# Performance work log

Measured on AMD Instinct MI355X. Metric: run time of the kernel, lower is better.

## Reference

```python
import jax, jax.numpy as jnp
import numpy as np

NUM_HEADS = 4


def setup_inputs() -> dict:
    key = jax.random.key(0)
    ks = jax.random.split(key, 5)
    B, C, L = 8, 128, 2048
    x = jax.random.normal(ks[0], (B, C, L), dtype=jnp.float32)
    # Conv1d(C, 3C, 1) == per-position linear; weight [3C, C], bias [3C]
    w_qkv = jax.random.normal(ks[1], (3 * C, C), dtype=jnp.float32) * (1.0 / np.sqrt(C))
    b_qkv = jax.random.normal(ks[2], (3 * C,), dtype=jnp.float32) * 0.01
    w_proj = jax.random.normal(ks[3], (C, C), dtype=jnp.float32) * (1.0 / np.sqrt(C))
    b_proj = jax.random.normal(ks[4], (C,), dtype=jnp.float32) * 0.01
    return {"x": x, "w_qkv": w_qkv, "b_qkv": b_qkv, "w_proj": w_proj, "b_proj": b_proj}


def reference(x, w_qkv, b_qkv, w_proj, b_proj):
    B, C, L = x.shape
    H = NUM_HEADS
    D = C // H
    scale = D ** -0.5
    # 1x1 conv qkv projection: [B, 3C, L]
    qkv = jnp.einsum('oc,bcl->bol', w_qkv, x) + b_qkv[None, :, None]
    # reshape (B,3,H,D,L) -> permute to (3,B,H,L,D)
    qkv = qkv.reshape(B, 3, H, D, L).transpose(1, 0, 2, 4, 3)
    q, k, v = qkv[0], qkv[1], qkv[2]  # each [B, H, L, D]
    attn = jax.nn.softmax(jnp.einsum('bhld,bhmd->bhlm', q, k) * scale, axis=-1)
    out = jnp.einsum('bhlm,bhmd->bhld', attn, v)  # [B, H, L, D]
    out = out.transpose(0, 1, 3, 2).reshape(B, C, L)
    out = jnp.einsum('oc,bcl->bol', w_proj, out) + b_proj[None, :, None]
    return out + x
```

## Files before the change

kernel.cpp:

```cpp
#include <hip/hip_runtime.h>

#define Bsz 8
#define Cdim 128
#define Lseq 2048
#define NH 4
#define HD 32
#define BH 32
#define QSCALE (0.17677669529663687f * 1.4426950408889634f)

typedef __bf16 bf16x8 __attribute__((ext_vector_type(8)));
typedef float f32x4 __attribute__((ext_vector_type(4)));
typedef unsigned u32x4 __attribute__((ext_vector_type(4)));

__device__ __forceinline__ float fexp2(float x) {
#if __has_builtin(__builtin_amdgcn_exp2f)
    return __builtin_amdgcn_exp2f(x);
#else
    return __expf(x * 0.6931471805599453f);
#endif
}

__device__ __forceinline__ unsigned short f2bf(float f) {
    unsigned u = __builtin_bit_cast(unsigned, f);
    u += 0x7FFFu + ((u >> 16) & 1u);
    return (unsigned short)(u >> 16);
}

__device__ __forceinline__ unsigned pack_bf16(float a, float b) {
    return (unsigned)f2bf(a) | ((unsigned)f2bf(b) << 16);
}

__device__ __forceinline__ unsigned pack_bf16_rtz(float a, float b) {
    return __builtin_amdgcn_perm(__builtin_bit_cast(unsigned, b),
                                 __builtin_bit_cast(unsigned, a), 0x07060302u);
}

__device__ __forceinline__ float bf_lo(unsigned u) {
    return __builtin_bit_cast(float, u << 16);
}
__device__ __forceinline__ float bf_hi(unsigned u) {
    return __builtin_bit_cast(float, u & 0xFFFF0000u);
}

#define MFMA16(A, B, C) __builtin_amdgcn_mfma_f32_16x16x32_bf16((A), (B), (C), 0, 0, 0)

__global__ __launch_bounds__(256) void qkv_kernel(const float* __restrict__ x,
        const float* __restrict__ w, const float* __restrict__ bias,
        unsigned short* __restrict__ qh, unsigned short* __restrict__ kh,
        unsigned short* __restrict__ vh) {
    __shared__ __attribute__((aligned(16))) unsigned short T[64][132];
    int bid = blockIdx.x;
    int og3 = bid % 3;
    int lt  = (bid / 3) & 31;
    int b   = bid / 96;
    int l0 = lt * 64;
    int t = threadIdx.x;
    int lane = t & 63, wv = t >> 6;
    int m16 = lane & 15, quad = lane >> 4;

    bf16x8 af[2][4];
    float bs[2][4];
    #pragma unroll
    for (int os = 0; os < 2; os++) {
        int orow = og3 * 128 + os * 64 + wv * 16;
        #pragma unroll
        for (int ks = 0; ks < 4; ks++) {
            const float* p = w + (size_t)(orow + m16) * Cdim + ks * 32 + quad * 8;
            float4 f0 = *(const float4*)p;
            float4 f1 = *(const float4*)(p + 4);
            u32x4 u = {pack_bf16(f0.x, f0.y), pack_bf16(f0.z, f0.w),
                       pack_bf16(f1.x, f1.y), pack_bf16(f1.z, f1.w)};
            af[os][ks] = __builtin_bit_cast(bf16x8, u);
        }
        #pragma unroll
        for (int r = 0; r < 4; r++) bs[os][r] = bias[orow + quad * 4 + r];
    }

    {
        int ll = t & 63, cg = t >> 6;
        const float* xb = x + (size_t)b * Cdim * Lseq + l0 + ll;
        #pragma unroll
        for (int i = 0; i < 16; i++) {
            int c = cg * 32 + 2 * i;
            float f0 = xb[(size_t)c * Lseq];
            float f1 = xb[(size_t)(c + 1) * Lseq];
            *(unsigned*)&T[ll][c] = pack_bf16(f0, f1);
        }
    }
    __syncthreads();

    #pragma unroll
    for (int ns = 0; ns < 4; ns++) {
        bf16x8 bx[4];
        #pragma unroll
        for (int ks = 0; ks < 4; ks++)
            bx[ks] = *(const bf16x8*)(&T[ns * 16 + m16][ks * 32 + quad * 8]);
        int l = l0 + ns * 16 + m16;
        #pragma unroll
        for (int os = 0; os < 2; os++) {
            f32x4 acc = {0.f, 0.f, 0.f, 0.f};
            #pragma unroll
            for (int ks = 0; ks < 4; ks++) acc = MFMA16(af[os][ks], bx[ks], acc);
            int oq = os * 64 + wv * 16 + quad * 4;
            if (og3 == 0) {
                int h = oq >> 5, d0 = oq & 31;
                uint2 u;
                u.x = pack_bf16((acc[0] + bs[os][0]) * QSCALE, (acc[1] + bs[os][1]) * QSCALE);
                u.y = pack_bf16((acc[2] + bs[os][2]) * QSCALE, (acc[3] + bs[os][3]) * QSCALE);
                *(uint2*)(qh + ((size_t)(b * NH + h) * Lseq + l) * HD + d0) = u;
            } else if (og3 == 1) {
                int h = oq >> 5, d0 = oq & 31;
                uint2 u;
                u.x = pack_bf16(acc[0] + bs[os][0], acc[1] + bs[os][1]);
                u.y = pack_bf16(acc[2] + bs[os][2], acc[3] + bs[os][3]);
                *(uint2*)(kh + ((size_t)(b * NH + h) * Lseq + l) * HD + d0) = u;
            } else {
                int kc = l >> 6, kk = l & 63;
                int half = kk >> 5, k32 = kk & 31;
                int q_, j_;
                if (k32 < 16) { q_ = k32 >> 2; j_ = k32 & 3; }
                else          { q_ = (k32 - 16) >> 2; j_ = 4 + ((k32 - 16) & 3); }
                int pos = half * 32 + q_ * 8 + j_;
                #pragma unroll
                for (int r = 0; r < 4; r++) {
                    int o = oq + r, h = o >> 5, d = o & 31;
                    vh[(((size_t)(b * NH + h) * 32 + kc) * HD + d) * 64 + pos] =
                        f2bf(acc[r] + bs[os][r]);
                }
            }
        }
    }
}

__global__ __launch_bounds__(256) void attn_kernel(
        const unsigned short* __restrict__ qh, const unsigned short* __restrict__ kh,
        const unsigned short* __restrict__ vh, unsigned short* __restrict__ oo) {
    __shared__ __attribute__((aligned(16))) char smem[22528];

    int bid = blockIdx.x;
    int xcd  = bid & 7;
    int rest = bid >> 3;
    int qt = rest & 31;
    int g  = rest >> 5;
    int bh = xcd + 8 * g;

    int lane = threadIdx.x & 63;
    int wv   = threadIdx.x >> 6;
    int m16  = lane & 15;
    int quad = lane >> 4;
    int l0 = qt * 64;

    bf16x8 qf[4];
    #pragma unroll
    for (int qs = 0; qs < 4; qs++)
        qf[qs] = *(const bf16x8*)(qh + ((size_t)bh * Lseq + l0 + qs * 16 + m16) * HD + quad * 8);

    f32x4 oacc[4][2];
    float sacc[4];
    #pragma unroll
    for (int qs = 0; qs < 4; qs++) {
        oacc[qs][0] = f32x4{0.f, 0.f, 0.f, 0.f};
        oacc[qs][1] = f32x4{0.f, 0.f, 0.f, 0.f};
        sacc[qs]    = 0.f;
    }
    f32x4 zero = {0.f, 0.f, 0.f, 0.f};

    const unsigned short* kb = kh + (size_t)bh * Lseq * HD + m16 * HD + quad * 8;
    const unsigned short* vb = vh + (size_t)bh * 32 * HD * 64;
    int kbase = wv * 512;

    auto load_kv = [&](int chunk, bf16x8* kf, bf16x8* vf) {
        int k0 = kbase + chunk * 64;
        #pragma unroll
        for (int t = 0; t < 4; t++)
            kf[t] = *(const bf16x8*)(kb + (size_t)(k0 + 16 * t) * HD);
        const unsigned short* vch = vb + (size_t)(k0 >> 6) * (HD * 64);
        vf[0] = *(const bf16x8*)(vch + m16 * 64 + quad * 8);
        vf[1] = *(const bf16x8*)(vch + (16 + m16) * 64 + quad * 8);
        vf[2] = *(const bf16x8*)(vch + m16 * 64 + 32 + quad * 8);
        vf[3] = *(const bf16x8*)(vch + (16 + m16) * 64 + 32 + quad * 8);
    };

    auto compute = [&](const bf16x8* kf, const bf16x8* vf) {
        #pragma unroll
        for (int qs = 0; qs < 4; qs++) {
            f32x4 s0 = MFMA16(kf[0], qf[qs], zero);
            f32x4 s1 = MFMA16(kf[1], qf[qs], zero);
            f32x4 s2 = MFMA16(kf[2], qf[qs], zero);
            f32x4 s3 = MFMA16(kf[3], qf[qs], zero);
            float p00 = fexp2(s0[0]), p01 = fexp2(s0[1]), p02 = fexp2(s0[2]), p03 = fexp2(s0[3]);
            float p10 = fexp2(s1[0]), p11 = fexp2(s1[1]), p12 = fexp2(s1[2]), p13 = fexp2(s1[3]);
            float p20 = fexp2(s2[0]), p21 = fexp2(s2[1]), p22 = fexp2(s2[2]), p23 = fexp2(s2[3]);
            float p30 = fexp2(s3[0]), p31 = fexp2(s3[1]), p32 = fexp2(s3[2]), p33 = fexp2(s3[3]);
            float r0 = (p00 + p01) + (p02 + p03);
            float r1 = (p10 + p11) + (p12 + p13);
            float r2 = (p20 + p21) + (p22 + p23);
            float r3 = (p30 + p31) + (p32 + p33);
            sacc[qs] += (r0 + r1) + (r2 + r3);
            u32x4 lo = {pack_bf16_rtz(p00, p01), pack_bf16_rtz(p02, p03),
                        pack_bf16_rtz(p10, p11), pack_bf16_rtz(p12, p13)};
            u32x4 hi = {pack_bf16_rtz(p20, p21), pack_bf16_rtz(p22, p23),
                        pack_bf16_rtz(p30, p31), pack_bf16_rtz(p32, p33)};
            bf16x8 pfL = __builtin_bit_cast(bf16x8, lo);
            bf16x8 pfH = __builtin_bit_cast(bf16x8, hi);
            oacc[qs][0] = MFMA16(vf[0], pfL, oacc[qs][0]);
            oacc[qs][1] = MFMA16(vf[1], pfL, oacc[qs][1]);
            oacc[qs][0] = MFMA16(vf[2], pfH, oacc[qs][0]);
            oacc[qs][1] = MFMA16(vf[3], pfH, oacc[qs][1]);
        }
    };

    bf16x8 kA[4], vA[4], kB[4], vB[4];
    load_kv(0, kA, vA);
    load_kv(1, kB, vB);
    compute(kA, vA); load_kv(2, kA, vA);
    compute(kB, vB); load_kv(3, kB, vB);
    compute(kA, vA); load_kv(4, kA, vA);
    compute(kB, vB); load_kv(5, kB, vB);
    compute(kA, vA); load_kv(6, kA, vA);
    compute(kB, vB); load_kv(7, kB, vB);
    compute(kA, vA);
    compute(kB, vB);

    unsigned* red_o = (unsigned*)smem;
    float* red_l = (float*)(smem + 18432);
    #pragma unroll
    for (int qs = 0; qs < 4; qs++) {
        int row = qs * 16 + m16;
        unsigned* rw = red_o + (size_t)(wv * 64 + row) * 18;
        *(uint2*)(rw + 2 * quad) =
            make_uint2(pack_bf16_rtz(oacc[qs][0][0], oacc[qs][0][1]),
                       pack_bf16_rtz(oacc[qs][0][2], oacc[qs][0][3]));
        *(uint2*)(rw + 8 + 2 * quad) =
            make_uint2(pack_bf16_rtz(oacc[qs][1][0], oacc[qs][1][1]),
                       pack_bf16_rtz(oacc[qs][1][2], oacc[qs][1][3]));
        red_l[(wv * 64 + row) * 4 + quad] = sacc[qs];
    }
    __syncthreads();

    int q = threadIdx.x >> 2;
    int s4 = (threadIdx.x & 3) * 4;
    float a8[8] = {0.f, 0.f, 0.f, 0.f, 0.f, 0.f, 0.f, 0.f};
    float lt = 0.f;
    #pragma unroll
    for (int w = 0; w < 4; w++) {
        const unsigned* rr = red_o + (size_t)(w * 64 + q) * 18 + s4;
        uint2 ua = *(const uint2*)(rr);
        uint2 ub = *(const uint2*)(rr + 2);
        a8[0] += bf_lo(ua.x); a8[1] += bf_hi(ua.x);
        a8[2] += bf_lo(ua.y); a8[3] += bf_hi(ua.y);
        a8[4] += bf_lo(ub.x); a8[5] += bf_hi(ub.x);
        a8[6] += bf_lo(ub.y); a8[7] += bf_hi(ub.y);
        float4 lv = *(const float4*)(red_l + (size_t)(w * 64 + q) * 4);
        lt += (lv.x + lv.y) + (lv.z + lv.w);
    }
    float inv = 1.0f / lt;
    int d0 = (threadIdx.x & 3) * 8;
    uint4 u;
    u.x = pack_bf16(a8[0] * inv, a8[1] * inv);
    u.y = pack_bf16(a8[2] * inv, a8[3] * inv);
    u.z = pack_bf16(a8[4] * inv, a8[5] * inv);
    u.w = pack_bf16(a8[6] * inv, a8[7] * inv);
    *(uint4*)(oo + ((size_t)bh * Lseq + l0 + q) * HD + d0) = u;
}

__global__ __launch_bounds__(256) void proj_kernel(const float* __restrict__ wp,
        const unsigned short* __restrict__ oo, const float* __restrict__ bias,
        const float* __restrict__ x, float* __restrict__ out) {
    int bid = blockIdx.x;
    int ot = bid & 1;
    int nt = bid >> 1;
    int n0 = nt * 32;
    int t = threadIdx.x;
    int lane = t & 63;
    int wv = t >> 6;
    int m16 = lane & 15, quad = lane >> 4;
    int o0 = ot * 64 + wv * 16;

    bf16x8 af[4];
    #pragma unroll
    for (int ks = 0; ks < 4; ks++) {
        const float* p = wp + (size_t)(o0 + m16) * Cdim + ks * 32 + quad * 8;
        float4 f0 = *(const float4*)p;
        float4 f1 = *(const float4*)(p + 4);
        u32x4 u = {pack_bf16(f0.x, f0.y), pack_bf16(f0.z, f0.w),
                   pack_bf16(f1.x, f1.y), pack_bf16(f1.z, f1.w)};
        af[ks] = __builtin_bit_cast(bf16x8, u);
    }
    float bs[4];
    #pragma unroll
    for (int r = 0; r < 4; r++) bs[r] = bias[o0 + quad * 4 + r];
    int oq = o0 + quad * 4;

    #pragma unroll
    for (int lt2 = 0; lt2 < 2; lt2++) {
        int n = n0 + lt2 * 16 + m16;
        int b = n >> 11, l = n & (Lseq - 1);
        bf16x8 bx[4];
        #pragma unroll
        for (int ks = 0; ks < 4; ks++)
            bx[ks] = *(const bf16x8*)(oo + ((size_t)(b * NH + ks) * Lseq + l) * HD + quad * 8);
        f32x4 acc = {0.f, 0.f, 0.f, 0.f};
        #pragma unroll
        for (int ks = 0; ks < 4; ks++) acc = MFMA16(af[ks], bx[ks], acc);
        #pragma unroll
        for (int r = 0; r < 4; r++) {
            size_t xi = ((size_t)b * Cdim + oq + r) * Lseq + l;
            out[xi] = acc[r] + bs[r] + x[xi];
        }
    }
}

extern "C" void kernel_launch(void* const* d_in, const int* in_sizes, int n_in,
                              void* d_out, int out_size, void* d_ws, size_t ws_size,
                              hipStream_t stream) {
    const float* x      = (const float*)d_in[0];
    const float* w_qkv  = (const float*)d_in[1];
    const float* b_qkv  = (const float*)d_in[2];
    const float* w_proj = (const float*)d_in[3];
    const float* b_proj = (const float*)d_in[4];
    float* out = (float*)d_out;

    const size_t E = (size_t)BH * Lseq * HD;
    unsigned short* qh = (unsigned short*)d_ws;
    unsigned short* kh = qh + E;
    unsigned short* vh = kh + E;
    unsigned short* oo = vh + E;

    qkv_kernel<<<dim3(768), dim3(256), 0, stream>>>(x, w_qkv, b_qkv, qh, kh, vh);
    attn_kernel<<<dim3(1024), dim3(256), 0, stream>>>(qh, kh, vh, oo);
    proj_kernel<<<dim3(1024), dim3(256), 0, stream>>>(w_proj, oo, b_proj, x, out);
}
```

Before: 114.9 us.

## Double attention query tile to 128 rows and remap qkv blocks across XCDs

Each attention block now handles 128 query rows instead of 64. Every K/V fragment loaded from global memory feeds twice as many score and PV MFMAs, which halves the grid to 512 blocks. The cross-wave reduction buffer grows to 48KB, and launch_bounds(256,2) is added to hold occupancy despite doubled accumulator registers. The qkv kernel's block index is also remapped so the three output groups for a tile sit on the same XCD, for L2 locality. The risks are register pressure or spills, and fewer blocks to fill the CUs.

```diff
diff --git a/kernel.cpp b/kernel.cpp
--- a/kernel.cpp
+++ b/kernel.cpp
@@ -50,9 +50,13 @@
         unsigned short* __restrict__ vh) {
     __shared__ __attribute__((aligned(16))) unsigned short T[64][132];
     int bid = blockIdx.x;
-    int og3 = bid % 3;
-    int lt  = (bid / 3) & 31;
-    int b   = bid / 96;
+    int xcd = bid & 7;
+    int s   = bid >> 3;
+    int og3 = s % 3;
+    int u_  = s / 3;
+    int trio = u_ * 8 + xcd;
+    int lt  = trio & 31;
+    int b   = trio >> 5;
     int l0 = lt * 64;
     int t = threadIdx.x;
     int lane = t & 63, wv = t >> 6;
@@ -132,37 +136,42 @@
     }
 }
 
-__global__ __launch_bounds__(256) void attn_kernel(
+__global__ __launch_bounds__(256, 2) void attn_kernel(
         const unsigned short* __restrict__ qh, const unsigned short* __restrict__ kh,
         const unsigned short* __restrict__ vh, unsigned short* __restrict__ oo) {
-    __shared__ __attribute__((aligned(16))) char smem[22528];
+    __shared__ __attribute__((aligned(16))) char smem[49152];
 
     int bid = blockIdx.x;
     int xcd  = bid & 7;
     int rest = bid >> 3;
-    int qt = rest & 31;
-    int g  = rest >> 5;
+    int qt = rest & 15;
+    int g  = rest >> 4;
     int bh = xcd + 8 * g;
 
     int lane = threadIdx.x & 63;
     int wv   = threadIdx.x >> 6;
     int m16  = lane & 15;
     int quad = lane >> 4;
-    int l0 = qt * 64;
-
-    bf16x8 qf[4];
-    #pragma unroll
-    for (int qs = 0; qs < 4; qs++)
-        qf[qs] = *(const bf16x8*)(qh + ((size_t)bh * Lseq + l0 + qs * 16 + m16) * HD + quad * 8);
-
-    f32x4 oacc[4][2];
-    float sacc[4];
-    #pragma unroll
-    for (int qs = 0; qs < 4; qs++) {
-        oacc[qs][0] = f32x4{0.f, 0.f, 0.f, 0.f};
-        oacc[qs][1] = f32x4{0.f, 0.f, 0.f, 0.f};
-        sacc[qs]    = 0.f;
-    }
+    int l0 = qt * 128;
+
+    bf16x8 qf[2][4];
+    #pragma unroll
+    for (int qt2 = 0; qt2 < 2; qt2++)
+        #pragma unroll
+        for (int qs = 0; qs < 4; qs++)
+            qf[qt2][qs] = *(const bf16x8*)(
+                qh + ((size_t)bh * Lseq + l0 + qt2 * 64 + qs * 16 + m16) * HD + quad * 8);
+
+    f32x4 oacc[2][4][2];
+    float sacc[2][4];
+    #pragma unroll
+    for (int qt2 = 0; qt2 < 2; qt2++)
+        #pragma unroll
+        for (int qs = 0; qs < 4; qs++) {
+            oacc[qt2][qs][0] = f32x4{0.f, 0.f, 0.f, 0.f};
+            oacc[qt2][qs][1] = f32x4{0.f, 0.f, 0.f, 0.f};
+            sacc[qt2][qs]    = 0.f;
+        }
     f32x4 zero = {0.f, 0.f, 0.f, 0.f};
 
     const unsigned short* kb = kh + (size_t)bh * Lseq * HD + m16 * HD + quad * 8;
@@ -183,30 +192,33 @@
 
     auto compute = [&](const bf16x8* kf, const bf16x8* vf) {
         #pragma unroll
-        for (int qs = 0; qs < 4; qs++) {
-            f32x4 s0 = MFMA16(kf[0], qf[qs], zero);
-            f32x4 s1 = MFMA16(kf[1], qf[qs], zero);
-            f32x4 s2 = MFMA16(kf[2], qf[qs], zero);
-            f32x4 s3 = MFMA16(kf[3], qf[qs], zero);
-            float p00 = fexp2(s0[0]), p01 = fexp2(s0[1]), p02 = fexp2(s0[2]), p03 = fexp2(s0[3]);
-            float p10 = fexp2(s1[0]), p11 = fexp2(s1[1]), p12 = fexp2(s1[2]), p13 = fexp2(s1[3]);
-            float p20 = fexp2(s2[0]), p21 = fexp2(s2[1]), p22 = fexp2(s2[2]), p23 = fexp2(s2[3]);
-            float p30 = fexp2(s3[0]), p31 = fexp2(s3[1]), p32 = fexp2(s3[2]), p33 = fexp2(s3[3]);
-            float r0 = (p00 + p01) + (p02 + p03);
-            float r1 = (p10 + p11) + (p12 + p13);
-            float r2 = (p20 + p21) + (p22 + p23);
-            float r3 = (p30 + p31) + (p32 + p33);
-            sacc[qs] += (r0 + r1) + (r2 + r3);
-            u32x4 lo = {pack_bf16_rtz(p00, p01), pack_bf16_rtz(p02, p03),
-                        pack_bf16_rtz(p10, p11), pack_bf16_rtz(p12, p13)};
-            u32x4 hi = {pack_bf16_rtz(p20, p21), pack_bf16_rtz(p22, p23),
-                        pack_bf16_rtz(p30, p31), pack_bf16_rtz(p32, p33)};
-            bf16x8 pfL = __builtin_bit_cast(bf16x8, lo);
-            bf16x8 pfH = __builtin_bit_cast(bf16x8, hi);
-            oacc[qs][0] = MFMA16(vf[0], pfL, oacc[qs][0]);
-            oacc[qs][1] = MFMA16(vf[1], pfL, oacc[qs][1]);
-            oacc[qs][0] = MFMA16(vf[2], pfH, oacc[qs][0]);
-            oacc[qs][1] = MFMA16(vf[3], pfH, oacc[qs][1]);
+        for (int qt2 = 0; qt2 < 2; qt2++) {
+            #pragma unroll
+            for (int qs = 0; qs < 4; qs++) {
+                f32x4 s0 = MFMA16(kf[0], qf[qt2][qs], zero);
+                f32x4 s1 = MFMA16(kf[1], qf[qt2][qs], zero);
+                f32x4 s2 = MFMA16(kf[2], qf[qt2][qs], zero);
+                f32x4 s3 = MFMA16(kf[3], qf[qt2][qs], zero);
+                float p00 = fexp2(s0[0]), p01 = fexp2(s0[1]), p02 = fexp2(s0[2]), p03 = fexp2(s0[3]);
+                float p10 = fexp2(s1[0]), p11 = fexp2(s1[1]), p12 = fexp2(s1[2]), p13 = fexp2(s1[3]);
+                float p20 = fexp2(s2[0]), p21 = fexp2(s2[1]), p22 = fexp2(s2[2]), p23 = fexp2(s2[3]);
+                float p30 = fexp2(s3[0]), p31 = fexp2(s3[1]), p32 = fexp2(s3[2]), p33 = fexp2(s3[3]);
+                float r0 = (p00 + p01) + (p02 + p03);
+                float r1 = (p10 + p11) + (p12 + p13);
+                float r2 = (p20 + p21) + (p22 + p23);
+                float r3 = (p30 + p31) + (p32 + p33);
+                sacc[qt2][qs] += (r0 + r1) + (r2 + r3);
+                u32x4 lo = {pack_bf16_rtz(p00, p01), pack_bf16_rtz(p02, p03),
+                            pack_bf16_rtz(p10, p11), pack_bf16_rtz(p12, p13)};
+                u32x4 hi = {pack_bf16_rtz(p20, p21), pack_bf16_rtz(p22, p23),
+                            pack_bf16_rtz(p30, p31), pack_bf16_rtz(p32, p33)};
+                bf16x8 pfL = __builtin_bit_cast(bf16x8, lo);
+                bf16x8 pfH = __builtin_bit_cast(bf16x8, hi);
+                oacc[qt2][qs][0] = MFMA16(vf[0], pfL, oacc[qt2][qs][0]);
+                oacc[qt2][qs][1] = MFMA16(vf[1], pfL, oacc[qt2][qs][1]);
+                oacc[qt2][qs][0] = MFMA16(vf[2], pfH, oacc[qt2][qs][0]);
+                oacc[qt2][qs][1] = MFMA16(vf[3], pfH, oacc[qt2][qs][1]);
+            }
         }
     };
 
@@ -223,45 +235,59 @@
     compute(kB, vB);
 
     unsigned* red_o = (unsigned*)smem;
-    float* red_l = (float*)(smem + 18432);
-    #pragma unroll
-    for (int qs = 0; qs < 4; qs++) {
-        int row = qs * 16 + m16;
-        unsigned* rw = red_o + (size_t)(wv * 64 + row) * 18;
-        *(uint2*)(rw + 2 * quad) =
-            make_uint2(pack_bf16_rtz(oacc[qs][0][0], oacc[qs][0][1]),
-                       pack_bf16_rtz(oacc[qs][0][2], oacc[qs][0][3]));
-        *(uint2*)(rw + 8 + 2 * quad) =
-            make_uint2(pack_bf16_rtz(oacc[qs][1][0], oacc[qs][1][1]),
-                       pack_bf16_rtz(oacc[qs][1][2], oacc[qs][1][3]));
-        red_l[(wv * 64 + row) * 4 + quad] = sacc[qs];
-    }
+    float* red_l = (float*)(smem + 40960);
+    #pragma unroll
+    for (int qt2 = 0; qt2 < 2; qt2++)
+        #pragma unroll
+        for (int qs = 0; qs < 4; qs++) {
+            int row = qt2 * 64 + qs * 16 + m16;
+            unsigned* rw = red_o + (size_t)(wv * 128 + row) * 20;
+            *(uint2*)(rw + 2 * quad) =
+                make_uint2(pack_bf16_rtz(oacc[qt2][qs][0][0], oacc[qt2][qs][0][1]),
+                           pack_bf16_rtz(oacc[qt2][qs][0][2], oacc[qt2][qs][0][3]));
+            *(uint2*)(rw + 8 + 2 * quad) =
+                make_uint2(pack_bf16_rtz(oacc[qt2][qs][1][0], oacc[qt2][qs][1][1]),
+                           pack_bf16_rtz(oacc[qt2][qs][1][2], oacc[qt2][qs][1][3]));
+            red_l[(wv * 128 + row) * 4 + quad] = sacc[qt2][qs];
+        }
     __syncthreads();
 
-    int q = threadIdx.x >> 2;
-    int s4 = (threadIdx.x & 3) * 4;
-    float a8[8] = {0.f, 0.f, 0.f, 0.f, 0.f, 0.f, 0.f, 0.f};
-    float lt = 0.f;
+    int q = threadIdx.x >> 1;
+    int hcol = threadIdx.x & 1;
+    int s8 = hcol * 8;
+    float a16[16];
+    #pragma unroll
+    for (int i = 0; i < 16; i++) a16[i] = 0.f;
+    float ltot = 0.f;
     #pragma unroll
     for (int w = 0; w < 4; w++) {
-        const unsigned* rr = red_o + (size_t)(w * 64 + q) * 18 + s4;
-        uint2 ua = *(const uint2*)(rr);
-        uint2 ub = *(const uint2*)(rr + 2);
-        a8[0] += bf_lo(ua.x); a8[1] += bf_hi(ua.x);
-        a8[2] += bf_lo(ua.y); a8[3] += bf_hi(ua.y);
-        a8[4] += bf_lo(ub.x); a8[5] += bf_hi(ub.x);
-        a8[6] += bf_lo(ub.y); a8[7] += bf_hi(ub.y);
-        float4 lv = *(const float4*)(red_l + (size_t)(w * 64 + q) * 4);
-        lt += (lv.x + lv.y) + (lv.z + lv.w);
-    }
-    float inv = 1.0f / lt;
-    int d0 = (threadIdx.x & 3) * 8;
-    uint4 u;
-    u.x = pack_bf16(a8[0] * inv, a8[1] * inv);
-    u.y = pack_bf16(a8[2] * inv, a8[3] * inv);
-    u.z = pack_bf16(a8[4] * inv, a8[5] * inv);
-    u.w = pack_bf16(a8[6] * inv, a8[7] * inv);
-    *(uint4*)(oo + ((size_t)bh * Lseq + l0 + q) * HD + d0) = u;
+        const unsigned* rr = red_o + (size_t)(w * 128 + q) * 20 + s8;
+        uint4 ua = *(const uint4*)rr;
+        uint4 ub = *(const uint4*)(rr + 4);
+        a16[0]  += bf_lo(ua.x); a16[1]  += bf_hi(ua.x);
+        a16[2]  += bf_lo(ua.y); a16[3]  += bf_hi(ua.y);
+        a16[4]  += bf_lo(ua.z); a16[5]  += bf_hi(ua.z);
+        a16[6]  += bf_lo(ua.w); a16[7]  += bf_hi(ua.w);
+        a16[8]  += bf_lo(ub.x); a16[9]  += bf_hi(ub.x);
+        a16[10] += bf_lo(ub.y); a16[11] += bf_hi(ub.y);
+        a16[12] += bf_lo(ub.z); a16[13] += bf_hi(ub.z);
+        a16[14] += bf_lo(ub.w); a16[15] += bf_hi(ub.w);
+        float4 lv = *(const float4*)(red_l + (size_t)(w * 128 + q) * 4);
+        ltot += (lv.x + lv.y) + (lv.z + lv.w);
+    }
+    float inv = 1.0f / ltot;
+    uint4 u0, u1;
+    u0.x = pack_bf16(a16[0] * inv,  a16[1] * inv);
+    u0.y = pack_bf16(a16[2] * inv,  a16[3] * inv);
+    u0.z = pack_bf16(a16[4] * inv,  a16[5] * inv);
+    u0.w = pack_bf16(a16[6] * inv,  a16[7] * inv);
+    u1.x = pack_bf16(a16[8] * inv,  a16[9] * inv);
+    u1.y = pack_bf16(a16[10] * inv, a16[11] * inv);
+    u1.z = pack_bf16(a16[12] * inv, a16[13] * inv);
+    u1.w = pack_bf16(a16[14] * inv, a16[15] * inv);
+    unsigned short* op = oo + ((size_t)bh * Lseq + l0 + q) * HD + hcol * 16;
+    *(uint4*)op = u0;
+    *(uint4*)(op + 8) = u1;
 }
 
 __global__ __launch_bounds__(256) void proj_kernel(const float* __restrict__ wp,
@@ -328,6 +354,6 @@
     unsigned short* oo = vh + E;
 
     qkv_kernel<<<dim3(768), dim3(256), 0, stream>>>(x, w_qkv, b_qkv, qh, kh, vh);
-    attn_kernel<<<dim3(1024), dim3(256), 0, stream>>>(qh, kh, vh, oo);
+    attn_kernel<<<dim3(512), dim3(256), 0, stream>>>(qh, kh, vh, oo);
     proj_kernel<<<dim3(1024), dim3(256), 0, stream>>>(w_proj, oo, b_proj, x, out);
 }
```

New measurement: 108.6 us. 5.5% less time.

## Stage V through LDS for vectorized stores, shrink attention chunk, XCD-aware QKV mapping

Applied to the files above, without the earlier changes.

The QKV kernel now writes V tiles into shared memory and then emits 16-byte coalesced stores in the permuted layout, replacing scattered 2-byte global writes. Block indices are remapped so the three output groups of one tile share an XCD. The attention kernel processes 32-key chunks with half the fragment registers, sets launch bounds to request occupancy 4, and pads the reduction stride. The intent is to remove uncoalesced V stores and lower register pressure so more waves are resident, at the cost of more loop iterations and an extra barrier plus LDS use in QKV.

```diff
diff --git a/kernel.cpp b/kernel.cpp
--- a/kernel.cpp
+++ b/kernel.cpp
@@ -49,10 +49,15 @@
         unsigned short* __restrict__ qh, unsigned short* __restrict__ kh,
         unsigned short* __restrict__ vh) {
     __shared__ __attribute__((aligned(16))) unsigned short T[64][132];
+    __shared__ __attribute__((aligned(16))) unsigned short V2[64][132];
     int bid = blockIdx.x;
-    int og3 = bid % 3;
-    int lt  = (bid / 3) & 31;
-    int b   = bid / 96;
+    int xcd = bid & 7;
+    int s   = bid >> 3;
+    int og3 = s % 3;
+    int u_  = s / 3;
+    int trio = u_ * 8 + xcd;
+    int lt  = trio & 31;
+    int b   = trio >> 5;
     int l0 = lt * 64;
     int t = threadIdx.x;
     int lane = t & 63, wv = t >> 6;
@@ -115,27 +120,44 @@
                 u.y = pack_bf16(acc[2] + bs[os][2], acc[3] + bs[os][3]);
                 *(uint2*)(kh + ((size_t)(b * NH + h) * Lseq + l) * HD + d0) = u;
             } else {
-                int kc = l >> 6, kk = l & 63;
-                int half = kk >> 5, k32 = kk & 31;
-                int q_, j_;
-                if (k32 < 16) { q_ = k32 >> 2; j_ = k32 & 3; }
-                else          { q_ = (k32 - 16) >> 2; j_ = 4 + ((k32 - 16) & 3); }
-                int pos = half * 32 + q_ * 8 + j_;
-                #pragma unroll
-                for (int r = 0; r < 4; r++) {
-                    int o = oq + r, h = o >> 5, d = o & 31;
-                    vh[(((size_t)(b * NH + h) * 32 + kc) * HD + d) * 64 + pos] =
-                        f2bf(acc[r] + bs[os][r]);
-                }
+                int kk = l & 63;
+                uint2 u;
+                u.x = pack_bf16(acc[0] + bs[os][0], acc[1] + bs[os][1]);
+                u.y = pack_bf16(acc[2] + bs[os][2], acc[3] + bs[os][3]);
+                *(uint2*)&V2[kk][oq] = u;
             }
         }
     }
-}
-
-__global__ __launch_bounds__(256) void attn_kernel(
+
+    if (og3 == 2) {
+        __syncthreads();
+        int kc = l0 >> 6;
+        #pragma unroll
+        for (int s2 = 0; s2 < 4; s2++) {
+            int i = t + 256 * s2;
+            int o = i >> 3;
+            int pos0 = (i & 7) * 8;
+            int half = pos0 >> 5, qq = (pos0 & 31) >> 3;
+            int kb2 = half * 32 + qq * 4;
+            unsigned short e0 = V2[kb2 + 0][o], e1 = V2[kb2 + 1][o];
+            unsigned short e2 = V2[kb2 + 2][o], e3 = V2[kb2 + 3][o];
+            unsigned short e4 = V2[kb2 + 16][o], e5 = V2[kb2 + 17][o];
+            unsigned short e6 = V2[kb2 + 18][o], e7 = V2[kb2 + 19][o];
+            uint4 u;
+            u.x = (unsigned)e0 | ((unsigned)e1 << 16);
+            u.y = (unsigned)e2 | ((unsigned)e3 << 16);
+            u.z = (unsigned)e4 | ((unsigned)e5 << 16);
+            u.w = (unsigned)e6 | ((unsigned)e7 << 16);
+            int h = o >> 5, d = o & 31;
+            *(uint4*)(vh + (((size_t)(b * NH + h) * 32 + kc) * HD + d) * 64 + pos0) = u;
+        }
+    }
+}
+
+__global__ __launch_bounds__(256, 4) void attn_kernel(
         const unsigned short* __restrict__ qh, const unsigned short* __restrict__ kh,
         const unsigned short* __restrict__ vh, unsigned short* __restrict__ oo) {
-    __shared__ __attribute__((aligned(16))) char smem[22528];
+    __shared__ __attribute__((aligned(16))) char smem[24576];
 
     int bid = blockIdx.x;
     int xcd  = bid & 7;
@@ -153,7 +175,8 @@
     bf16x8 qf[4];
     #pragma unroll
     for (int qs = 0; qs < 4; qs++)
-        qf[qs] = *(const bf16x8*)(qh + ((size_t)bh * Lseq + l0 + qs * 16 + m16) * HD + quad * 8);
+        qf[qs] = *(const bf16x8*)(
+            qh + ((size_t)bh * Lseq + l0 + qs * 16 + m16) * HD + quad * 8);
 
     f32x4 oacc[4][2];
     float sacc[4];
@@ -170,15 +193,13 @@
     int kbase = wv * 512;
 
     auto load_kv = [&](int chunk, bf16x8* kf, bf16x8* vf) {
-        int k0 = kbase + chunk * 64;
-        #pragma unroll
-        for (int t = 0; t < 4; t++)
-            kf[t] = *(const bf16x8*)(kb + (size_t)(k0 + 16 * t) * HD);
-        const unsigned short* vch = vb + (size_t)(k0 >> 6) * (HD * 64);
+        int k0 = kbase + chunk * 32;
+        kf[0] = *(const bf16x8*)(kb + (size_t)k0 * HD);
+        kf[1] = *(const bf16x8*)(kb + (size_t)(k0 + 16) * HD);
+        const unsigned short* vch = vb + (size_t)(k0 >> 6) * (HD * 64)
+                                       + ((k0 >> 5) & 1) * 32;
         vf[0] = *(const bf16x8*)(vch + m16 * 64 + quad * 8);
         vf[1] = *(const bf16x8*)(vch + (16 + m16) * 64 + quad * 8);
-        vf[2] = *(const bf16x8*)(vch + m16 * 64 + 32 + quad * 8);
-        vf[3] = *(const bf16x8*)(vch + (16 + m16) * 64 + 32 + quad * 8);
     };
 
     auto compute = [&](const bf16x8* kf, const bf16x8* vf) {
@@ -186,48 +207,34 @@
         for (int qs = 0; qs < 4; qs++) {
             f32x4 s0 = MFMA16(kf[0], qf[qs], zero);
             f32x4 s1 = MFMA16(kf[1], qf[qs], zero);
-            f32x4 s2 = MFMA16(kf[2], qf[qs], zero);
-            f32x4 s3 = MFMA16(kf[3], qf[qs], zero);
             float p00 = fexp2(s0[0]), p01 = fexp2(s0[1]), p02 = fexp2(s0[2]), p03 = fexp2(s0[3]);
             float p10 = fexp2(s1[0]), p11 = fexp2(s1[1]), p12 = fexp2(s1[2]), p13 = fexp2(s1[3]);
-            float p20 = fexp2(s2[0]), p21 = fexp2(s2[1]), p22 = fexp2(s2[2]), p23 = fexp2(s2[3]);
-            float p30 = fexp2(s3[0]), p31 = fexp2(s3[1]), p32 = fexp2(s3[2]), p33 = fexp2(s3[3]);
-            float r0 = (p00 + p01) + (p02 + p03);
-            float r1 = (p10 + p11) + (p12 + p13);
-            float r2 = (p20 + p21) + (p22 + p23);
-            float r3 = (p30 + p31) + (p32 + p33);
-            sacc[qs] += (r0 + r1) + (r2 + r3);
+            sacc[qs] += ((p00 + p01) + (p02 + p03)) + ((p10 + p11) + (p12 + p13));
             u32x4 lo = {pack_bf16_rtz(p00, p01), pack_bf16_rtz(p02, p03),
                         pack_bf16_rtz(p10, p11), pack_bf16_rtz(p12, p13)};
-            u32x4 hi = {pack_bf16_rtz(p20, p21), pack_bf16_rtz(p22, p23),
-                        pack_bf16_rtz(p30, p31), pack_bf16_rtz(p32, p33)};
             bf16x8 pfL = __builtin_bit_cast(bf16x8, lo);
-            bf16x8 pfH = __builtin_bit_cast(bf16x8, hi);
             oacc[qs][0] = MFMA16(vf[0], pfL, oacc[qs][0]);
             oacc[qs][1] = MFMA16(vf[1], pfL, oacc[qs][1]);
-            oacc[qs][0] = MFMA16(vf[2], pfH, oacc[qs][0]);
-            oacc[qs][1] = MFMA16(vf[3], pfH, oacc[qs][1]);
         }
     };
 
-    bf16x8 kA[4], vA[4], kB[4], vB[4];
+    bf16x8 kA[2], vA[2], kB[2], vB[2];
     load_kv(0, kA, vA);
     load_kv(1, kB, vB);
-    compute(kA, vA); load_kv(2, kA, vA);
-    compute(kB, vB); load_kv(3, kB, vB);
-    compute(kA, vA); load_kv(4, kA, vA);
-    compute(kB, vB); load_kv(5, kB, vB);
-    compute(kA, vA); load_kv(6, kA, vA);
-    compute(kB, vB); load_kv(7, kB, vB);
-    compute(kA, vA);
-    compute(kB, vB);
+    #pragma unroll
+    for (int it = 0; it < 8; it++) {
+        compute(kA, vA);
+        if (it < 7) load_kv(2 * it + 2, kA, vA);
+        compute(kB, vB);
+        if (it < 7) load_kv(2 * it + 3, kB, vB);
+    }
 
     unsigned* red_o = (unsigned*)smem;
-    float* red_l = (float*)(smem + 18432);
+    float* red_l = (float*)(smem + 20480);
     #pragma unroll
     for (int qs = 0; qs < 4; qs++) {
         int row = qs * 16 + m16;
-        unsigned* rw = red_o + (size_t)(wv * 64 + row) * 18;
+        unsigned* rw = red_o + (size_t)(wv * 64 + row) * 20;
         *(uint2*)(rw + 2 * quad) =
             make_uint2(pack_bf16_rtz(oacc[qs][0][0], oacc[qs][0][1]),
                        pack_bf16_rtz(oacc[qs][0][2], oacc[qs][0][3]));
@@ -241,10 +248,10 @@
     int q = threadIdx.x >> 2;
     int s4 = (threadIdx.x & 3) * 4;
     float a8[8] = {0.f, 0.f, 0.f, 0.f, 0.f, 0.f, 0.f, 0.f};
-    float lt = 0.f;
+    float ltot = 0.f;
     #pragma unroll
     for (int w = 0; w < 4; w++) {
-        const unsigned* rr = red_o + (size_t)(w * 64 + q) * 18 + s4;
+        const unsigned* rr = red_o + (size_t)(w * 64 + q) * 20 + s4;
         uint2 ua = *(const uint2*)(rr);
         uint2 ub = *(const uint2*)(rr + 2);
         a8[0] += bf_lo(ua.x); a8[1] += bf_hi(ua.x);
@@ -252,9 +259,9 @@
         a8[4] += bf_lo(ub.x); a8[5] += bf_hi(ub.x);
         a8[6] += bf_lo(ub.y); a8[7] += bf_hi(ub.y);
         float4 lv = *(const float4*)(red_l + (size_t)(w * 64 + q) * 4);
-        lt += (lv.x + lv.y) + (lv.z + lv.w);
-    }
-    float inv = 1.0f / lt;
+        ltot += (lv.x + lv.y) + (lv.z + lv.w);
+    }
+    float inv = 1.0f / ltot;
     int d0 = (threadIdx.x & 3) * 8;
     uint4 u;
     u.x = pack_bf16(a8[0] * inv, a8[1] * inv);
```

Result: slower. 340.7 us (+196.6%).
